# Kernel optimization log

Hardware: AMD Instinct MI355X
Metric: run time of the kernel (lower is better)

## Reference

```python
import jax, jax.numpy as jnp
import numpy as np

NUM_CLASSES = 64
BASE_MARGIN = 0.1
ADAPTIVE_WEIGHT = 0.1
STAT_WEIGHT = 0.1


def setup_inputs() -> dict:
    key = jax.random.key(0)
    k1, k2 = jax.random.split(key)
    feats = jax.random.normal(k1, (4096, 512), dtype=jnp.float32)
    labels = jax.random.randint(k2, (4096,), 0, NUM_CLASSES, dtype=jnp.int64)
    return {"feats": feats, "labels": labels}


def _forward(feats, labels):
    N, D = feats.shape
    # pairwise euclidean distances (torch.cdist p=2), nan-safe sqrt
    sq = jnp.sum(feats * feats, axis=-1)                      # [N]
    d2 = sq[:, None] + sq[None, :] - 2.0 * (feats @ feats.T)  # [N,N]
    d2 = jnp.maximum(d2, 0.0)
    dist = jnp.sqrt(jnp.where(d2 > 0.0, d2, 1.0))
    dist = jnp.where(d2 > 0.0, dist, 0.0)

    # class stats (first-call EMA == batch stats), under stop_gradient (torch.no_grad)
    sg = jax.lax.stop_gradient(feats)
    counts = jax.ops.segment_sum(jnp.ones((N,), feats.dtype), labels, NUM_CLASSES)  # [C]
    denom = jnp.maximum(counts, 1.0)[:, None]
    cmean = jax.ops.segment_sum(sg, labels, NUM_CLASSES) / denom                    # [C,D]
    cmsq = jax.ops.segment_sum(sg * sg, labels, NUM_CLASSES) / denom                # [C,D]
    cvar = jnp.maximum(cmsq - cmean * cmean, 0.0)  # biased variance (unbiased=False)

    # statistical margin per sample: ||f_i - mean[y_i]|| * mean(var[y_i])
    diff = feats - cmean[labels]                               # grads flow via feats only
    center_dist2 = jnp.sum(diff * diff, axis=-1)
    center_dist = jnp.sqrt(jnp.where(center_dist2 > 0.0, center_dist2, 1.0))
    center_dist = jnp.where(center_dist2 > 0.0, center_dist, 0.0)
    uncertainty = jnp.mean(cvar, axis=-1)[labels]              # [N]
    stat_margin = center_dist * uncertainty

    same = labels[:, None] == labels[None, :]                  # [N,N]
    eye = jnp.eye(N, dtype=bool)
    pos_mask = same & ~eye                                     # matches pos_dist > 0 filter
    neg_mask = ~same

    big = jnp.asarray(1e30, dist.dtype)
    hardest_pos = jnp.max(jnp.where(pos_mask, dist, -big), axis=1)
    hardest_neg = jnp.min(jnp.where(neg_mask, dist, big), axis=1)
    pos_cnt = jnp.sum(pos_mask, axis=1).astype(dist.dtype)
    neg_cnt = jnp.sum(neg_mask, axis=1).astype(dist.dtype)
    mean_pos = jnp.sum(jnp.where(pos_mask, dist, 0.0), axis=1) / jnp.maximum(pos_cnt, 1.0)
    mean_neg = jnp.sum(jnp.where(neg_mask, dist, 0.0), axis=1) / jnp.maximum(neg_cnt, 1.0)

    final_margin = (BASE_MARGIN + ADAPTIVE_WEIGHT * (mean_neg - mean_pos)
                    + STAT_WEIGHT * stat_margin)
    per_sample = jax.nn.relu(hardest_pos - hardest_neg + final_margin)

    valid = (pos_cnt > 0) & (neg_cnt > 0)
    n_valid = jnp.sum(valid.astype(dist.dtype))
    loss = jnp.sum(jnp.where(valid, per_sample, 0.0)) / jnp.maximum(n_valid, 1.0)
    return jnp.where(n_valid > 0, loss, 0.0)


def reference(feats, labels):
    return _forward(feats, labels)
```

## Files before the change

### kernel.cpp

```cpp
#include <hip/hip_runtime.h>
#include <hip/hip_bf16.h>


#define NN 4096
#define DD 512
#define NCLS 64

typedef __bf16 bf16x8 __attribute__((ext_vector_type(8)));
typedef float f32x4 __attribute__((ext_vector_type(4)));

__device__ __forceinline__ void gload_lds16(const void* g, void* l) {
  __builtin_amdgcn_global_load_lds(
      (const __attribute__((address_space(1))) void*)g,
      (__attribute__((address_space(3))) void*)l, 16, 0, 0);
}

__global__ __launch_bounds__(512) void k_stats(
    const float* __restrict__ feats, const int* __restrict__ labels,
    float* __restrict__ counts, float* __restrict__ cmean,
    float* __restrict__ uncert) {
  __shared__ __align__(16) int slab[NN];
  __shared__ int list[NN];
  __shared__ int chunk_off[64];
  __shared__ int sM;
  __shared__ float sred[512];
  const int c = blockIdx.x;
  const int t = threadIdx.x;
  const int lane = t & 63;
  const int wv = t >> 6;
  for (int i = t; i < NN; i += 512) slab[i] = labels[i];
  __syncthreads();
  for (int ch = wv; ch < 64; ch += 8) {
    const unsigned long long m = __ballot(slab[ch * 64 + lane] == c);
    if (lane == 0) chunk_off[ch] = __popcll(m);
  }
  __syncthreads();
  if (wv == 0) {
    const int v = chunk_off[lane];
    int inc = v;
#pragma unroll
    for (int off = 1; off < 64; off <<= 1) {
      const int o = __shfl_up(inc, off);
      if (lane >= off) inc += o;
    }
    chunk_off[lane] = inc - v;
    if (lane == 63) sM = inc;
  }
  __syncthreads();
  const int M = sM;
  for (int ch = wv; ch < 64; ch += 8) {
    const bool my = (slab[ch * 64 + lane] == c);
    const unsigned long long m = __ballot(my);
    if (my) {
      const int pos = chunk_off[ch] + __popcll(m & ((1ULL << lane) - 1ULL));
      list[pos] = ch * 64 + lane;
    }
  }
  __syncthreads();
  float s1 = 0.f, s2 = 0.f;
  int m = 0;
  for (; m + 8 <= M; m += 8) {
    float v[8];
#pragma unroll
    for (int e = 0; e < 8; ++e) v[e] = feats[(size_t)list[m + e] * DD + t];
#pragma unroll
    for (int e = 0; e < 8; ++e) { s1 += v[e]; s2 += v[e] * v[e]; }
  }
  for (; m < M; ++m) {
    const float v = feats[(size_t)list[m] * DD + t];
    s1 += v; s2 += v * v;
  }
  const float den = fmaxf((float)M, 1.f);
  const float mean = s1 / den;
  const float var = fmaxf(s2 / den - mean * mean, 0.f);
  cmean[c * DD + t] = mean;
  sred[t] = var;
  __syncthreads();
  for (int s = 256; s > 0; s >>= 1) {
    if (t < s) sred[t] += sred[t + s];
    __syncthreads();
  }
  if (t == 0) {
    uncert[c] = sred[0] / (float)DD;
    counts[c] = (float)M;
  }
}

__global__ __launch_bounds__(256) void k_row(
    const float* __restrict__ feats, const int* __restrict__ labels,
    const float* __restrict__ cmean, unsigned short* __restrict__ fb,
    float* __restrict__ sqb, float* __restrict__ cd2) {
  const int w = threadIdx.x >> 6;
  const int lane = threadIdx.x & 63;
  const int row = blockIdx.x * 4 + w;
  const int lab = labels[row];
  const float4* fr = (const float4*)(feats + (size_t)row * DD);
  const float4* cm = (const float4*)(cmean + (size_t)lab * DD);
  float sq = 0.f, c2 = 0.f;
  unsigned int ob[4];
#pragma unroll
  for (int h = 0; h < 2; ++h) {
    const float4 f = fr[lane * 2 + h];
    const float4 cv = cm[lane * 2 + h];
    const float fe[4] = {f.x, f.y, f.z, f.w};
    const float ce[4] = {cv.x, cv.y, cv.z, cv.w};
    unsigned short us[4];
#pragma unroll
    for (int e = 0; e < 4; ++e) {
      const __bf16 b = (__bf16)fe[e];
      const float bf = (float)b;
      sq += bf * bf;
      const float dd = fe[e] - ce[e];
      c2 += dd * dd;
      us[e] = __builtin_bit_cast(unsigned short, b);
    }
    ob[h * 2]     = (unsigned int)us[0] | ((unsigned int)us[1] << 16);
    ob[h * 2 + 1] = (unsigned int)us[2] | ((unsigned int)us[3] << 16);
  }
  *(uint4*)(fb + (size_t)row * DD + lane * 8) = make_uint4(ob[0], ob[1], ob[2], ob[3]);
#pragma unroll
  for (int off = 32; off > 0; off >>= 1) {
    sq += __shfl_xor(sq, off);
    c2 += __shfl_xor(c2, off);
  }
  if (lane == 0) {
    sqb[row] = sq;
    cd2[row] = c2;
  }
}

__global__ __launch_bounds__(256, 3) void k_gemm(
    const unsigned short* __restrict__ fb, const float* __restrict__ sqb,
    const int* __restrict__ labels,
    float* __restrict__ php, float* __restrict__ phn,
    float* __restrict__ pst, float* __restrict__ pss) {
  __shared__ __align__(16) unsigned short sA[128 * 64];
  __shared__ __align__(16) unsigned short sB[128 * 64];
  __shared__ int s_labi[128], s_labj[128];
  __shared__ float s_sqi[128], s_sqj[128];

  const int bid = blockIdx.x;
  const int swz = ((bid & 7) << 7) + (bid >> 3);
  const int ib = swz >> 5, jb = swz & 31;
  const int ibase = ib << 7, jbase = jb << 7;
  const int t = threadIdx.x;
  const int lane = t & 63;
  const int w = t >> 6;
  const int wm = w >> 1, wn = w & 1;
  const int rin = lane & 15;
  const int g4 = lane >> 4;
  const int swzbyte = (g4 ^ (rin & 7)) << 4;
  const int abase = ((wm << 6) + rin) << 7;
  const int bbase = ((wn << 6) + rin) << 7;

  if (t < 128) {
    s_labi[t] = labels[ibase + t];
    s_labj[t] = labels[jbase + t];
    s_sqi[t] = sqb[ibase + t];
    s_sqj[t] = sqb[jbase + t];
  }

  f32x4 acc[4][4];
#pragma unroll
  for (int mi = 0; mi < 4; ++mi)
#pragma unroll
    for (int nj = 0; nj < 4; ++nj)
      acc[mi][nj] = (f32x4){0.f, 0.f, 0.f, 0.f};

  for (int kt = 0; kt < 8; ++kt) {
#pragma unroll
    for (int r = 0; r < 4; ++r) {
      const int q = (r << 8) + t;
      const int row = q >> 3;
      const int ch = q & 7;
      const int ksrc = (kt << 6) + ((ch ^ (row & 7)) << 3);
      gload_lds16(fb + (size_t)(ibase + row) * DD + ksrc, &sA[q << 3]);
      gload_lds16(fb + (size_t)(jbase + row) * DD + ksrc, &sB[q << 3]);
    }
    __syncthreads();
    const char* A = (const char*)sA;
    const char* B = (const char*)sB;
#pragma unroll
    for (int ks = 0; ks < 2; ++ks) {
      bf16x8 af[4], bg[4];
#pragma unroll
      for (int mi = 0; mi < 4; ++mi)
        af[mi] = *(const bf16x8*)(A + abase + (mi << 11) + (swzbyte ^ (ks << 6)));
#pragma unroll
      for (int nj = 0; nj < 4; ++nj)
        bg[nj] = *(const bf16x8*)(B + bbase + (nj << 11) + (swzbyte ^ (ks << 6)));
#pragma unroll
      for (int mi = 0; mi < 4; ++mi)
#pragma unroll
        for (int nj = 0; nj < 4; ++nj)
          acc[mi][nj] = __builtin_amdgcn_mfma_f32_16x16x32_bf16(
              af[mi], bg[nj], acc[mi][nj], 0, 0, 0);
    }
    __syncthreads();
  }

  float qj[4];
  int lj[4];
#pragma unroll
  for (int nj = 0; nj < 4; ++nj) {
    const int cl = (wn << 6) + (nj << 4) + rin;
    qj[nj] = s_sqj[cl];
    lj[nj] = s_labj[cl];
  }
  const int jidx = (jb << 1) + wn;
#pragma unroll
  for (int mi = 0; mi < 4; ++mi) {
#pragma unroll
    for (int r = 0; r < 4; ++r) {
      const int rl = (wm << 6) + (mi << 4) + (g4 << 2) + r;
      const float qi = s_sqi[rl];
      const int li = s_labi[rl];
      float hp = 0.f, hn = 1e30f, st = 0.f, ss = 0.f;
#pragma unroll
      for (int nj = 0; nj < 4; ++nj) {
        const float g = acc[mi][nj][r];
        float d2 = qi + qj[nj] - 2.f * g;
        d2 = fmaxf(d2, 0.f);
        const float dist = sqrtf(d2);
        const bool same = (li == lj[nj]);
        const float dp = same ? dist : 0.f;
        hp = fmaxf(hp, dp);
        hn = fminf(hn, same ? 1e30f : dist);
        st += dist;
        ss += dp;
      }
#pragma unroll
      for (int off = 1; off < 16; off <<= 1) {
        hp = fmaxf(hp, __shfl_xor(hp, off));
        hn = fminf(hn, __shfl_xor(hn, off));
        st += __shfl_xor(st, off);
        ss += __shfl_xor(ss, off);
      }
      if (rin == 0) {
        const int grow = ibase + rl;
        php[jidx * NN + grow] = hp;
        phn[jidx * NN + grow] = hn;
        pst[jidx * NN + grow] = st;
        pss[jidx * NN + grow] = ss;
      }
    }
  }
}

__global__ __launch_bounds__(256) void k_fin1(
    const int* __restrict__ labels, const float* __restrict__ counts,
    const float* __restrict__ uncert, const float* __restrict__ cd2,
    const float* __restrict__ php, const float* __restrict__ phn,
    const float* __restrict__ pst, const float* __restrict__ pss,
    float* __restrict__ pf) {
  const int t = threadIdx.x;
  const int row = blockIdx.x * 256 + t;
  float hp = 0.f, hn = 1e30f, st = 0.f, ss = 0.f;
#pragma unroll 8
  for (int j = 0; j < 64; ++j) {
    hp = fmaxf(hp, php[j * NN + row]);
    hn = fminf(hn, phn[j * NN + row]);
    st += pst[j * NN + row];
    ss += pss[j * NN + row];
  }
  const int lab = labels[row];
  const float cnt = counts[lab];
  const float pos = cnt - 1.f;
  const float neg = (float)NN - cnt;
  const float mean_pos = ss / fmaxf(pos, 1.f);
  const float mean_neg = (st - ss) / fmaxf(neg, 1.f);
  const float c2 = cd2[row];
  const float cdist = (c2 > 0.f) ? sqrtf(c2) : 0.f;
  const float margin = 0.1f + 0.1f * (mean_neg - mean_pos) + 0.1f * (cdist * uncert[lab]);
  const float ps = fmaxf(hp - hn + margin, 0.f);
  const bool valid = (pos > 0.f) && (neg > 0.f);
  float s = valid ? ps : 0.f;
  float c = valid ? 1.f : 0.f;
#pragma unroll
  for (int off = 1; off < 64; off <<= 1) {
    s += __shfl_xor(s, off);
    c += __shfl_xor(c, off);
  }
  __shared__ float ws1[4], ws2[4];
  const int lane = t & 63;
  const int wv = t >> 6;
  if (lane == 0) { ws1[wv] = s; ws2[wv] = c; }
  __syncthreads();
  if (t == 0) {
    pf[2 * blockIdx.x] = ws1[0] + ws1[1] + ws1[2] + ws1[3];
    pf[2 * blockIdx.x + 1] = ws2[0] + ws2[1] + ws2[2] + ws2[3];
  }
}

__global__ __launch_bounds__(64) void k_fin2(const float* __restrict__ pf,
                                             float* __restrict__ out) {
  const int t = threadIdx.x;
  float s = 0.f, c = 0.f;
  if (t < 16) { s = pf[2 * t]; c = pf[2 * t + 1]; }
#pragma unroll
  for (int off = 1; off < 16; off <<= 1) {
    s += __shfl_xor(s, off);
    c += __shfl_xor(c, off);
  }
  if (t == 0) out[0] = (c > 0.f) ? (s / fmaxf(c, 1.f)) : 0.f;
}

extern "C" void kernel_launch(void* const* d_in, const int* in_sizes, int n_in,
                              void* d_out, int out_size, void* d_ws, size_t ws_size,
                              hipStream_t stream) {
  (void)in_sizes; (void)n_in; (void)out_size; (void)ws_size;
  const float* feats = (const float*)d_in[0];
  const int* labels = (const int*)d_in[1];
  char* w = (char*)d_ws;
  float* counts = (float*)(w + 0);
  float* uncert = (float*)(w + 1024);
  float* sqb    = (float*)(w + 2048);
  float* cd2    = (float*)(w + 18432);
  float* pf     = (float*)(w + 34816);
  float* cmean  = (float*)(w + 36864);
  unsigned short* fb = (unsigned short*)(w + 167936);
  float* php = (float*)(w + 4362240);
  float* phn = (float*)(w + 5410816);
  float* pst = (float*)(w + 6459392);
  float* pss = (float*)(w + 7507968);

  k_stats<<<dim3(64), dim3(512), 0, stream>>>(feats, labels, counts, cmean, uncert);
  k_row<<<dim3(1024), dim3(256), 0, stream>>>(feats, labels, cmean, fb, sqb, cd2);
  k_gemm<<<dim3(1024), dim3(256), 0, stream>>>(fb, sqb, labels, php, phn, pst, pss);
  k_fin1<<<dim3(16), dim3(256), 0, stream>>>(labels, counts, uncert, cd2,
                                             php, phn, pst, pss, pf);
  k_fin2<<<dim3(1), dim3(64), 0, stream>>>(pf, (float*)d_out);
}
```

Measured before the change: 63.22 us.

## Double-buffer GEMM LDS tiles with async prefetch and remap block-to-tile assignment

The GEMM main loop now uses two LDS buffers for the A and B tiles. The next k-tile is fetched with global_load_lds while MFMAs run on the current one, and manual vmcnt and lgkmcnt waits with raw barriers replace the full __syncthreads. The block-to-tile mapping is changed so each XCD covers a contiguous 8x16 region, which is meant to improve L2 reuse. LDS use doubles and the occupancy hint of 3 is dropped, which may reduce resident blocks per CU.

Result: no change. 64.04 us (+1.3%).

```diff
diff --git a/kernel.cpp b/kernel.cpp
--- a/kernel.cpp
+++ b/kernel.cpp
@@ -129,19 +129,21 @@
   }
 }
 
-__global__ __launch_bounds__(256, 3) void k_gemm(
+__global__ __launch_bounds__(256) void k_gemm(
     const unsigned short* __restrict__ fb, const float* __restrict__ sqb,
     const int* __restrict__ labels,
     float* __restrict__ php, float* __restrict__ phn,
     float* __restrict__ pst, float* __restrict__ pss) {
-  __shared__ __align__(16) unsigned short sA[128 * 64];
-  __shared__ __align__(16) unsigned short sB[128 * 64];
+  __shared__ __align__(16) unsigned short sA[2][128 * 64];
+  __shared__ __align__(16) unsigned short sB[2][128 * 64];
   __shared__ int s_labi[128], s_labj[128];
   __shared__ float s_sqi[128], s_sqj[128];
 
   const int bid = blockIdx.x;
-  const int swz = ((bid & 7) << 7) + (bid >> 3);
-  const int ib = swz >> 5, jb = swz & 31;
+  const int xcd = bid & 7;
+  const int w8 = bid >> 3;
+  const int ib = ((xcd & 3) << 3) + (w8 & 7);
+  const int jb = ((xcd >> 2) << 4) + (w8 >> 3);
   const int ibase = ib << 7, jbase = jb << 7;
   const int t = threadIdx.x;
   const int lane = t & 63;
@@ -160,6 +162,20 @@
     s_sqj[t] = sqb[jbase + t];
   }
 
+  const unsigned short* gA[4];
+  const unsigned short* gB[4];
+  int lo[4];
+#pragma unroll
+  for (int r = 0; r < 4; ++r) {
+    const int q = (r << 8) + t;
+    const int row = q >> 3;
+    const int ch = q & 7;
+    const int koff = (ch ^ (row & 7)) << 3;
+    gA[r] = fb + (size_t)(ibase + row) * DD + koff;
+    gB[r] = fb + (size_t)(jbase + row) * DD + koff;
+    lo[r] = q << 3;
+  }
+
   f32x4 acc[4][4];
 #pragma unroll
   for (int mi = 0; mi < 4; ++mi)
@@ -167,19 +183,28 @@
     for (int nj = 0; nj < 4; ++nj)
       acc[mi][nj] = (f32x4){0.f, 0.f, 0.f, 0.f};
 
+#pragma unroll
+  for (int r = 0; r < 4; ++r) {
+    gload_lds16(gA[r], &sA[0][lo[r]]);
+    gload_lds16(gB[r], &sB[0][lo[r]]);
+  }
+
+#pragma unroll
   for (int kt = 0; kt < 8; ++kt) {
-#pragma unroll
-    for (int r = 0; r < 4; ++r) {
-      const int q = (r << 8) + t;
-      const int row = q >> 3;
-      const int ch = q & 7;
-      const int ksrc = (kt << 6) + ((ch ^ (row & 7)) << 3);
-      gload_lds16(fb + (size_t)(ibase + row) * DD + ksrc, &sA[q << 3]);
-      gload_lds16(fb + (size_t)(jbase + row) * DD + ksrc, &sB[q << 3]);
-    }
-    __syncthreads();
-    const char* A = (const char*)sA;
-    const char* B = (const char*)sB;
+    const int cur = kt & 1;
+    if (kt < 7) {
+#pragma unroll
+      for (int r = 0; r < 4; ++r) {
+        gload_lds16(gA[r] + ((kt + 1) << 6), &sA[cur ^ 1][lo[r]]);
+        gload_lds16(gB[r] + ((kt + 1) << 6), &sB[cur ^ 1][lo[r]]);
+      }
+      asm volatile("s_waitcnt vmcnt(8)" ::: "memory");
+    } else {
+      asm volatile("s_waitcnt vmcnt(0)" ::: "memory");
+    }
+    __builtin_amdgcn_s_barrier();
+    const char* A = (const char*)sA[cur];
+    const char* B = (const char*)sB[cur];
 #pragma unroll
     for (int ks = 0; ks < 2; ++ks) {
       bf16x8 af[4], bg[4];
@@ -196,7 +221,10 @@
           acc[mi][nj] = __builtin_amdgcn_mfma_f32_16x16x32_bf16(
               af[mi], bg[nj], acc[mi][nj], 0, 0, 0);
     }
-    __syncthreads();
+    if (kt < 7) {
+      asm volatile("s_waitcnt lgkmcnt(0)" ::: "memory");
+      __builtin_amdgcn_s_barrier();
+    }
   }
 
   float qj[4];
```
